# Performance work log

Measured on AMD Instinct MI355X. Metric: run time of the kernel, lower is better.

Reference implementation:

```python
import jax, jax.numpy as jnp
import numpy as np

NEG_SLOPE = 0.01  # F.leaky_relu default


def gcn_conv(x, src, dst, norm, W, b, n_nodes):
    """PyG-style GCNConv: h = x @ W; out[i] = sum_{(j->i)} norm_e * h[j] + b.
    src/dst/norm already include self-loops and symmetric D^-1/2 A D^-1/2 weights."""
    h = x @ W                                   # [N, out]
    msgs = h[src] * norm[:, None]               # [E+N, out] gather
    out = jax.ops.segment_sum(msgs, dst, num_segments=n_nodes)  # scatter-add
    return out + b


def _build_norm(edge_idx, n_nodes):
    """Add self-loops and compute symmetric GCN normalization coefficients."""
    loops = jnp.arange(n_nodes, dtype=edge_idx.dtype)
    src = jnp.concatenate([edge_idx[0], loops])
    dst = jnp.concatenate([edge_idx[1], loops])
    deg = jax.ops.segment_sum(jnp.ones_like(dst, dtype=jnp.float32), dst,
                              num_segments=n_nodes)
    dinv = jnp.where(deg > 0, jax.lax.rsqrt(jnp.maximum(deg, 1.0)), 0.0)
    norm = dinv[src] * dinv[dst]
    return src, dst, norm


def setup_inputs() -> dict:
    key = jax.random.key(0)
    k = jax.random.split(key, 8)
    N, E, nfeat, nhid = 50000, 800000, 64, 64
    x = jax.random.normal(k[0], (N, nfeat), dtype=jnp.float32)
    edge_idx = jax.random.randint(k[1], (2, E), 0, N, dtype=jnp.int32)
    # inverted dropout mask, p=0.5 -> values in {0, 2}
    drop_mask = (jax.random.uniform(k[2], (N, nhid)) >= 0.5).astype(jnp.float32) * 2.0
    # glorot-style GCNConv weights + zero bias (PyG defaults)
    s1 = (6.0 / (nfeat + nhid)) ** 0.5
    s2 = (6.0 / (nhid + nhid // 2)) ** 0.5
    W1 = jax.random.uniform(k[3], (nfeat, nhid), minval=-s1, maxval=s1, dtype=jnp.float32)
    b1 = jnp.zeros((nhid,), dtype=jnp.float32)
    W2 = jax.random.uniform(k[4], (nhid, nhid // 2), minval=-s2, maxval=s2, dtype=jnp.float32)
    b2 = jnp.zeros((nhid // 2,), dtype=jnp.float32)
    return {"x": x, "edge_idx": edge_idx, "drop_mask": drop_mask,
            "W1": W1, "b1": b1, "W2": W2, "b2": b2}


def reference(x, edge_idx, drop_mask, W1, b1, W2, b2):
    n_nodes = x.shape[0]
    src, dst, norm = _build_norm(edge_idx, n_nodes)
    h = jax.nn.leaky_relu(gcn_conv(x, src, dst, norm, W1, b1, n_nodes), NEG_SLOPE)
    h = h * drop_mask  # F.dropout(p=0.5) with precomputed inverted mask
    out = jax.nn.leaky_relu(gcn_conv(h, src, dst, norm, W2, b2, n_nodes), NEG_SLOPE)
    return out
```

## Files before the change

kernel.cpp:

```cpp
#include <hip/hip_runtime.h>
#include <hip/hip_fp16.h>

#define NEG_SLOPE 0.01f
typedef unsigned int uint;
typedef unsigned short u16;

#define NBK 256
#define CHUNK 4096
#define KPT 16
#define GROWS 16

__device__ __forceinline__ float wbits(uint rec) {
    u16 b = (u16)(rec >> 16);
    __half h;
    *reinterpret_cast<u16*>(&h) = b;
    return __half2float(h);
}

__device__ __forceinline__ void acc8(uint4 v, float w, float* a) {
    float2 f;
    f = __half22float2(*reinterpret_cast<__half2*>(&v.x)); a[0] = fmaf(f.x, w, a[0]); a[1] = fmaf(f.y, w, a[1]);
    f = __half22float2(*reinterpret_cast<__half2*>(&v.y)); a[2] = fmaf(f.x, w, a[2]); a[3] = fmaf(f.y, w, a[3]);
    f = __half22float2(*reinterpret_cast<__half2*>(&v.z)); a[4] = fmaf(f.x, w, a[4]); a[5] = fmaf(f.y, w, a[5]);
    f = __half22float2(*reinterpret_cast<__half2*>(&v.w)); a[6] = fmaf(f.x, w, a[6]); a[7] = fmaf(f.y, w, a[7]);
}

__device__ __forceinline__ void unpack8(uint4 v, float* s) {
    float2 f;
    f = __half22float2(*reinterpret_cast<__half2*>(&v.x)); s[0] = f.x; s[1] = f.y;
    f = __half22float2(*reinterpret_cast<__half2*>(&v.y)); s[2] = f.x; s[3] = f.y;
    f = __half22float2(*reinterpret_cast<__half2*>(&v.z)); s[4] = f.x; s[5] = f.y;
    f = __half22float2(*reinterpret_cast<__half2*>(&v.w)); s[6] = f.x; s[7] = f.y;
}

__global__ __launch_bounds__(256) void gemm1_hist(const float* __restrict__ X,
                                                  const float* __restrict__ W,
                                                  __half* __restrict__ H, int N,
                                                  const int* __restrict__ dst,
                                                  uint* __restrict__ hist, int E,
                                                  int gblocks) {
    __shared__ uint lh[NBK];
    if ((int)blockIdx.x >= gblocks) {
        int cb = (int)blockIdx.x - gblocks;
        int t = threadIdx.x;
        lh[t] = 0u;
        __syncthreads();
        int base = cb * CHUNK;
#pragma unroll
        for (int r = 0; r < 4; ++r) {
            int e4 = base + r * 1024 + t * 4;
            if (e4 + 3 < E) {
                int4 d = *(const int4*)(dst + e4);
                atomicAdd(&lh[((uint)d.x) >> 8], 1u);
                atomicAdd(&lh[((uint)d.y) >> 8], 1u);
                atomicAdd(&lh[((uint)d.z) >> 8], 1u);
                atomicAdd(&lh[((uint)d.w) >> 8], 1u);
            } else {
                for (int e = e4; e < E && e < e4 + 4; ++e)
                    atomicAdd(&lh[((uint)dst[e]) >> 8], 1u);
            }
        }
        __syncthreads();
        hist[(size_t)cb * NBK + t] = lh[t];
        return;
    }
    int lane = threadIdx.x & 63;
    int wv = threadIdx.x >> 6;
    float wc[64];
#pragma unroll
    for (int k = 0; k < 64; ++k) wc[k] = W[k * 64 + lane];
    size_t plane = (size_t)(lane >> 5) * ((size_t)N * 32);
    int c = lane & 31;
    int rowBase = ((int)blockIdx.x * 4 + wv) * GROWS;
    for (int g = 0; g < GROWS; g += 4) {
        int r0 = __builtin_amdgcn_readfirstlane(rowBase + g);
        if (r0 >= N) return;
        int e1 = min(r0 + 1, N - 1), e2 = min(r0 + 2, N - 1), e3 = min(r0 + 3, N - 1);
        const float* x0 = X + (size_t)r0 * 64;
        const float* x1 = X + (size_t)e1 * 64;
        const float* x2 = X + (size_t)e2 * 64;
        const float* x3 = X + (size_t)e3 * 64;
        float a0 = 0.f, a1 = 0.f, a2 = 0.f, a3 = 0.f;
        float b0 = 0.f, b1 = 0.f, b2 = 0.f, b3 = 0.f;
#pragma unroll
        for (int k = 0; k < 64; k += 2) {
            a0 = fmaf(x0[k], wc[k], a0); b0 = fmaf(x0[k + 1], wc[k + 1], b0);
            a1 = fmaf(x1[k], wc[k], a1); b1 = fmaf(x1[k + 1], wc[k + 1], b1);
            a2 = fmaf(x2[k], wc[k], a2); b2 = fmaf(x2[k + 1], wc[k + 1], b2);
            a3 = fmaf(x3[k], wc[k], a3); b3 = fmaf(x3[k + 1], wc[k + 1], b3);
        }
        H[plane + (size_t)r0 * 32 + c] = __float2half(a0 + b0);
        if (r0 + 1 < N) H[plane + (size_t)(r0 + 1) * 32 + c] = __float2half(a1 + b1);
        if (r0 + 2 < N) H[plane + (size_t)(r0 + 2) * 32 + c] = __float2half(a2 + b2);
        if (r0 + 3 < N) H[plane + (size_t)(r0 + 3) * 32 + c] = __float2half(a3 + b3);
    }
}

__global__ __launch_bounds__(256) void scan_hist(uint* __restrict__ hist,
                                                 uint* __restrict__ buckTotal,
                                                 int nchunks) {
    __shared__ uint lds[256];
    int b = blockIdx.x;
    int t = threadIdx.x;
    uint carry = 0;
    for (int c0 = 0; c0 < nchunks; c0 += 256) {
        int c = c0 + t;
        uint v = (c < nchunks) ? hist[(size_t)c * NBK + b] : 0u;
        lds[t] = v;
        __syncthreads();
        for (int off = 1; off < 256; off <<= 1) {
            uint u = (t >= off) ? lds[t - off] : 0u;
            __syncthreads();
            lds[t] += u;
            __syncthreads();
        }
        uint incl = lds[t];
        if (c < nchunks) hist[(size_t)c * NBK + b] = carry + incl - v;
        uint tot = lds[255];
        __syncthreads();
        carry += tot;
    }
    if (t == 0) buckTotal[b] = carry;
}

__global__ __launch_bounds__(256) void partition_edges(const int* __restrict__ src,
                                                       const int* __restrict__ dst,
                                                       const uint* __restrict__ hist,
                                                       const uint* __restrict__ buckTotal,
                                                       uint* __restrict__ staging,
                                                       int E) {
    __shared__ uint lh[NBK];
    __shared__ uint sc[NBK];
    __shared__ uint runbase[NBK];
    int t = threadIdx.x;
    lh[t] = 0u;
    uint tot = buckTotal[t];
    sc[t] = tot;
    __syncthreads();
    for (int off = 1; off < NBK; off <<= 1) {
        uint u = (t >= off) ? sc[t - off] : 0u;
        __syncthreads();
        sc[t] += u;
        __syncthreads();
    }
    int base = blockIdx.x * CHUNK;
    uint rec[KPT], rb[KPT], rk[KPT];
#pragma unroll
    for (int r = 0; r < 4; ++r) {
        int e4 = base + r * 1024 + t * 4;
        if (e4 + 3 < E) {
            int4 s = *(const int4*)(src + e4);
            int4 d = *(const int4*)(dst + e4);
            int k = r * 4;
            rb[k + 0] = ((uint)d.x) >> 8; rec[k + 0] = (uint)s.x | (((uint)d.x & 255u) << 16);
            rb[k + 1] = ((uint)d.y) >> 8; rec[k + 1] = (uint)s.y | (((uint)d.y & 255u) << 16);
            rb[k + 2] = ((uint)d.z) >> 8; rec[k + 2] = (uint)s.z | (((uint)d.z & 255u) << 16);
            rb[k + 3] = ((uint)d.w) >> 8; rec[k + 3] = (uint)s.w | (((uint)d.w & 255u) << 16);
            rk[k + 0] = atomicAdd(&lh[rb[k + 0]], 1u);
            rk[k + 1] = atomicAdd(&lh[rb[k + 1]], 1u);
            rk[k + 2] = atomicAdd(&lh[rb[k + 2]], 1u);
            rk[k + 3] = atomicAdd(&lh[rb[k + 3]], 1u);
        } else {
            for (int j = 0; j < 4; ++j) {
                int e = e4 + j;
                int k = r * 4 + j;
                if (e < E) {
                    uint s = (uint)src[e], d = (uint)dst[e];
                    rb[k] = d >> 8;
                    rec[k] = s | ((d & 255u) << 16);
                    rk[k] = atomicAdd(&lh[rb[k]], 1u);
                } else rb[k] = 0xFFFFFFFFu;
            }
        }
    }
    __syncthreads();
    runbase[t] = (sc[t] - tot) + hist[(size_t)blockIdx.x * NBK + t];
    __syncthreads();
#pragma unroll
    for (int k = 0; k < KPT; ++k)
        if (rb[k] != 0xFFFFFFFFu)
            staging[runbase[rb[k]] + rk[k]] = rec[k];
}

__global__ __launch_bounds__(256) void build_csr(const uint* __restrict__ staging,
                                                 const uint* __restrict__ buckTotal,
                                                 u16* __restrict__ srcIdx,
                                                 uint* __restrict__ offs,
                                                 float* __restrict__ dinv,
                                                 int N, int nbuck) {
    __shared__ uint nh[256];
    __shared__ uint nstart[256];
    __shared__ u16 rankbuf[8192];
    __shared__ u16 outbuf[8192];
    int b = blockIdx.x;
    int t = threadIdx.x;
    uint tot = buckTotal[t];
    nstart[t] = tot;
    __syncthreads();
    for (int off = 1; off < NBK; off <<= 1) {
        uint u = (t >= off) ? nstart[t - off] : 0u;
        __syncthreads();
        nstart[t] += u;
        __syncthreads();
    }
    uint endb = nstart[b];
    uint base = endb - buckTotal[b];
    __syncthreads();
    uint T = endb - base;
    nh[t] = 0u;
    __syncthreads();
    for (uint i = t; i < T; i += 256) {
        uint rec = staging[base + i];
        rankbuf[i] = (u16)atomicAdd(&nh[(rec >> 16) & 255u], 1u);
    }
    __syncthreads();
    uint deg = nh[t];
    nstart[t] = deg;
    __syncthreads();
    for (int off = 1; off < 256; off <<= 1) {
        uint u = (t >= off) ? nstart[t - off] : 0u;
        __syncthreads();
        nstart[t] += u;
        __syncthreads();
    }
    uint excl = nstart[t] - deg;
    __syncthreads();
    nstart[t] = excl;
    __syncthreads();
    for (uint i = t; i < T; i += 256) {
        uint rec = staging[base + i];
        outbuf[nstart[(rec >> 16) & 255u] + rankbuf[i]] = (u16)(rec & 0xFFFFu);
    }
    __syncthreads();
    for (uint i = t; i < T; i += 256) srcIdx[base + i] = outbuf[i];
    int node = b * 256 + t;
    if (node < N) {
        offs[node] = base + excl;
        dinv[node] = rsqrtf((float)(deg + 1u));
    }
    if (b == nbuck - 1 && t == 0) offs[N] = endb;
}

__global__ __launch_bounds__(256) void fill_pack(const u16* __restrict__ srcIdx,
                                                 const float* __restrict__ dinv,
                                                 uint* __restrict__ packed, int E) {
    int i4 = (blockIdx.x * 256 + threadIdx.x) * 4;
    if (i4 + 3 < E) {
        ushort4 s = *(const ushort4*)(srcIdx + i4);
        uint4 o;
        __half h0 = __float2half(dinv[s.x]);
        __half h1 = __float2half(dinv[s.y]);
        __half h2 = __float2half(dinv[s.z]);
        __half h3 = __float2half(dinv[s.w]);
        o.x = (uint)s.x | ((uint)*reinterpret_cast<u16*>(&h0) << 16);
        o.y = (uint)s.y | ((uint)*reinterpret_cast<u16*>(&h1) << 16);
        o.z = (uint)s.z | ((uint)*reinterpret_cast<u16*>(&h2) << 16);
        o.w = (uint)s.w | ((uint)*reinterpret_cast<u16*>(&h3) << 16);
        *(uint4*)(packed + i4) = o;
    } else {
        for (int i = i4; i < E; ++i) {
            __half h = __float2half(dinv[srcIdx[i]]);
            packed[i] = (uint)srcIdx[i] | ((uint)*reinterpret_cast<u16*>(&h) << 16);
        }
    }
}

__global__ __launch_bounds__(256) void agg1(const __half* __restrict__ h,
                                            const uint* __restrict__ offs,
                                            const uint* __restrict__ packed,
                                            const float* __restrict__ dinv,
                                            const float* __restrict__ b,
                                            const float* __restrict__ mask,
                                            __half* __restrict__ outp,
                                            int N, int nb1) {
    int half = ((int)blockIdx.x >= nb1) ? 1 : 0;
    int blk = (int)blockIdx.x - half * nb1;
    int node = blk * 4 + (threadIdx.x >> 6);
    if (node >= N) return;
    int lane = threadIdx.x & 63;
    int r = lane >> 2;
    int q = lane & 3;
    const uint4* h8 = (const uint4*)(h + (size_t)half * N * 32);
    uint beg = offs[node], end = offs[node + 1];
    float a[8] = {0.f, 0.f, 0.f, 0.f, 0.f, 0.f, 0.f, 0.f};
    uint p = beg + (uint)r;
    for (; p + 16 < end; p += 32) {
        uint e0 = packed[p], e1 = packed[p + 16];
        uint4 v0 = h8[(size_t)(e0 & 0xFFFFu) * 4 + q];
        uint4 v1 = h8[(size_t)(e1 & 0xFFFFu) * 4 + q];
        acc8(v0, wbits(e0), a);
        acc8(v1, wbits(e1), a);
    }
    for (; p < end; p += 16) {
        uint e0 = packed[p];
        uint4 v0 = h8[(size_t)(e0 & 0xFFFFu) * 4 + q];
        acc8(v0, wbits(e0), a);
    }
#pragma unroll
    for (int i = 0; i < 8; ++i) {
        a[i] += __shfl_xor(a[i], 4, 64);
        a[i] += __shfl_xor(a[i], 8, 64);
        a[i] += __shfl_xor(a[i], 16, 64);
        a[i] += __shfl_xor(a[i], 32, 64);
    }
    if (r == 0) {
        float dv = dinv[node];
        float dv2 = dv * dv;
        float s[8];
        unpack8(h8[(size_t)node * 4 + q], s);
        const float4* b4 = (const float4*)b;
        float4 bv0 = b4[half * 8 + q * 2];
        float4 bv1 = b4[half * 8 + q * 2 + 1];
        const float4* m4 = (const float4*)mask;
        float4 mv0 = m4[(size_t)node * 16 + half * 8 + q * 2];
        float4 mv1 = m4[(size_t)node * 16 + half * 8 + q * 2 + 1];
        float bb[8] = {bv0.x, bv0.y, bv0.z, bv0.w, bv1.x, bv1.y, bv1.z, bv1.w};
        float mm[8] = {mv0.x, mv0.y, mv0.z, mv0.w, mv1.x, mv1.y, mv1.z, mv1.w};
        uint4 o;
        uint* op = (uint*)&o;
#pragma unroll
        for (int i = 0; i < 4; ++i) {
            float v0 = a[2 * i] * dv + s[2 * i] * dv2 + bb[2 * i];
            float v1 = a[2 * i + 1] * dv + s[2 * i + 1] * dv2 + bb[2 * i + 1];
            v0 = (v0 > 0.f) ? v0 : NEG_SLOPE * v0;
            v1 = (v1 > 0.f) ? v1 : NEG_SLOPE * v1;
            v0 *= mm[2 * i]; v1 *= mm[2 * i + 1];
            __half2 hh = __floats2half2_rn(v0, v1);
            op[i] = *reinterpret_cast<uint*>(&hh);
        }
        ((uint4*)(outp + (size_t)half * N * 32))[(size_t)node * 4 + q] = o;
    }
}

__global__ __launch_bounds__(256) void gemm64x32(const __half* __restrict__ Xh,
                                                 const float* __restrict__ W,
                                                 __half* __restrict__ H, int N) {
    int lane = threadIdx.x & 63;
    int col = lane & 31;
    int wv = threadIdx.x >> 6;
    size_t N32 = (size_t)N * 32;
    float wc[64];
#pragma unroll
    for (int k = 0; k < 64; ++k) wc[k] = W[k * 32 + col];
    int rowBase = ((int)blockIdx.x * 4 + wv) * GROWS;
    for (int g = 0; g < GROWS; g += 4) {
        int r0 = __builtin_amdgcn_readfirstlane(rowBase + g);
        if (r0 >= N) return;
        int e1 = min(r0 + 1, N - 1), e2 = min(r0 + 2, N - 1), e3 = min(r0 + 3, N - 1);
        float a0 = 0.f, a1 = 0.f, a2 = 0.f, a3 = 0.f;
        float b0 = 0.f, b1 = 0.f, b2 = 0.f, b3 = 0.f;
#pragma unroll
        for (int pl = 0; pl < 2; ++pl) {
            const uint* x0 = (const uint*)(Xh + pl * N32 + (size_t)r0 * 32);
            const uint* x1 = (const uint*)(Xh + pl * N32 + (size_t)e1 * 32);
            const uint* x2 = (const uint*)(Xh + pl * N32 + (size_t)e2 * 32);
            const uint* x3 = (const uint*)(Xh + pl * N32 + (size_t)e3 * 32);
#pragma unroll
            for (int kk = 0; kk < 16; ++kk) {
                uint u0 = x0[kk], u1 = x1[kk], u2 = x2[kk], u3 = x3[kk];
                float2 f0 = __half22float2(*reinterpret_cast<__half2*>(&u0));
                float2 f1 = __half22float2(*reinterpret_cast<__half2*>(&u1));
                float2 f2 = __half22float2(*reinterpret_cast<__half2*>(&u2));
                float2 f3 = __half22float2(*reinterpret_cast<__half2*>(&u3));
                int k0 = pl * 32 + 2 * kk;
                a0 = fmaf(f0.x, wc[k0], a0); b0 = fmaf(f0.y, wc[k0 + 1], b0);
                a1 = fmaf(f1.x, wc[k0], a1); b1 = fmaf(f1.y, wc[k0 + 1], b1);
                a2 = fmaf(f2.x, wc[k0], a2); b2 = fmaf(f2.y, wc[k0 + 1], b2);
                a3 = fmaf(f3.x, wc[k0], a3); b3 = fmaf(f3.y, wc[k0 + 1], b3);
            }
        }
        if (lane < 32) {
            H[(size_t)r0 * 32 + col] = __float2half(a0 + b0);
            if (r0 + 1 < N) H[(size_t)(r0 + 1) * 32 + col] = __float2half(a1 + b1);
            if (r0 + 2 < N) H[(size_t)(r0 + 2) * 32 + col] = __float2half(a2 + b2);
            if (r0 + 3 < N) H[(size_t)(r0 + 3) * 32 + col] = __float2half(a3 + b3);
        }
    }
}

__global__ __launch_bounds__(256) void agg2(const __half* __restrict__ h,
                                            const uint* __restrict__ offs,
                                            const uint* __restrict__ packed,
                                            const float* __restrict__ dinv,
                                            const float* __restrict__ b,
                                            float* __restrict__ outp, int N) {
    int node = (int)blockIdx.x * 4 + (threadIdx.x >> 6);
    if (node >= N) return;
    int lane = threadIdx.x & 63;
    int r = lane >> 2;
    int q = lane & 3;
    const uint4* h8 = (const uint4*)h;
    uint beg = offs[node], end = offs[node + 1];
    float a[8] = {0.f, 0.f, 0.f, 0.f, 0.f, 0.f, 0.f, 0.f};
    uint p = beg + (uint)r;
    for (; p + 16 < end; p += 32) {
        uint e0 = packed[p], e1 = packed[p + 16];
        uint4 v0 = h8[(size_t)(e0 & 0xFFFFu) * 4 + q];
        uint4 v1 = h8[(size_t)(e1 & 0xFFFFu) * 4 + q];
        acc8(v0, wbits(e0), a);
        acc8(v1, wbits(e1), a);
    }
    for (; p < end; p += 16) {
        uint e0 = packed[p];
        uint4 v0 = h8[(size_t)(e0 & 0xFFFFu) * 4 + q];
        acc8(v0, wbits(e0), a);
    }
#pragma unroll
    for (int i = 0; i < 8; ++i) {
        a[i] += __shfl_xor(a[i], 4, 64);
        a[i] += __shfl_xor(a[i], 8, 64);
        a[i] += __shfl_xor(a[i], 16, 64);
        a[i] += __shfl_xor(a[i], 32, 64);
    }
    if (r == 0) {
        float dv = dinv[node];
        float dv2 = dv * dv;
        float s[8];
        unpack8(h8[(size_t)node * 4 + q], s);
        float4 bv0 = ((const float4*)b)[q * 2];
        float4 bv1 = ((const float4*)b)[q * 2 + 1];
        float bb[8] = {bv0.x, bv0.y, bv0.z, bv0.w, bv1.x, bv1.y, bv1.z, bv1.w};
        float o[8];
#pragma unroll
        for (int i = 0; i < 8; ++i) {
            float v = a[i] * dv + s[i] * dv2 + bb[i];
            o[i] = (v > 0.f) ? v : NEG_SLOPE * v;
        }
        float4* outv = (float4*)outp;
        outv[(size_t)node * 8 + q * 2]     = make_float4(o[0], o[1], o[2], o[3]);
        outv[(size_t)node * 8 + q * 2 + 1] = make_float4(o[4], o[5], o[6], o[7]);
    }
}

extern "C" void kernel_launch(void* const* d_in, const int* in_sizes, int n_in,
                              void* d_out, int out_size, void* d_ws, size_t ws_size,
                              hipStream_t stream) {
    const float* x    = (const float*)d_in[0];
    const int*   ei   = (const int*)d_in[1];
    const float* mask = (const float*)d_in[2];
    const float* W1   = (const float*)d_in[3];
    const float* b1   = (const float*)d_in[4];
    const float* W2   = (const float*)d_in[5];
    const float* b2   = (const float*)d_in[6];
    float* out = (float*)d_out;

    const int N = in_sizes[0] / 64;
    const int E = in_sizes[1] / 2;
    const int* src = ei;
    const int* dst = ei + E;

    const int nbuck  = (N + 255) >> 8;
    const int chunks = (E + CHUNK - 1) / CHUNK;
    const int gblocks = (N + 4 * GROWS - 1) / (4 * GROWS);
    const int nb1 = (N + 3) / 4;

    char* w = (char*)d_ws;
    uint*  hist      = (uint*)w;    w += (size_t)chunks * NBK * 4;
    uint*  buckTotal = (uint*)w;    w += NBK * 4;
    w = (char*)(((size_t)w + 15) & ~15ull);
    uint*  offs      = (uint*)w;    w += (size_t)(N + 1) * 4;
    w = (char*)(((size_t)w + 15) & ~15ull);
    float* dinv      = (float*)w;   w += (size_t)N * 4;
    uint*  staging   = (uint*)w;    w += (size_t)E * 4;
    u16*   srcIdx    = (u16*)w;     w += (((size_t)E * 2 + 15) & ~15ull);
    uint*  packed    = (uint*)w;    w += (size_t)E * 4;
    __half* h1       = (__half*)w;  w += (size_t)N * 64 * 2;
    __half* hpost    = (__half*)w;  w += (size_t)N * 64 * 2;
    __half* h2       = h1;

    gemm1_hist<<<gblocks + chunks, 256, 0, stream>>>(x, W1, h1, N, dst, hist, E, gblocks);
    scan_hist<<<NBK, 256, 0, stream>>>(hist, buckTotal, chunks);
    partition_edges<<<chunks, 256, 0, stream>>>(src, dst, hist, buckTotal, staging, E);
    build_csr<<<nbuck, 256, 0, stream>>>(staging, buckTotal, srcIdx, offs, dinv, N, nbuck);
    fill_pack<<<(E + 1023) / 1024, 256, 0, stream>>>(srcIdx, dinv, packed, E);

    agg1<<<2 * nb1, 256, 0, stream>>>(h1, offs, packed, dinv, b1, mask, hpost, N, nb1);

    gemm64x32<<<gblocks, 256, 0, stream>>>(hpost, W2, h2, N);
    agg2<<<nb1, 256, 0, stream>>>(h2, offs, packed, dinv, b2, out, N);
}
```

Measured before the change: 137.1 us.

## Assign one node per 4-lane group in aggregation kernels instead of per wavefront

Both aggregation kernels now map each 4-lane group to one destination node, so a wavefront handles 16 nodes, where before one wavefront covered a single node. Each group walks its node's edge list sequentially with 4-way unrolled gathers, and the cross-lane shuffle reduction is gone. The goal is to stop wasting lanes, since average degree is about 17, so the 16-edge-strided loop left many lanes idle, and to remove the reduction overhead. In exchange, lanes in a wavefront diverge when their nodes have different degrees, and gather coalescing changes.

Measured after the change: 116.0 us (median of 2 runs). 1.18x faster.

```diff
diff --git a/kernel.cpp b/kernel.cpp
--- a/kernel.cpp
+++ b/kernel.cpp
@@ -272,48 +272,47 @@
                                             const float* __restrict__ b,
                                             const float* __restrict__ mask,
                                             __half* __restrict__ outp,
-                                            int N, int nb1) {
-    int half = ((int)blockIdx.x >= nb1) ? 1 : 0;
-    int blk = (int)blockIdx.x - half * nb1;
-    int node = blk * 4 + (threadIdx.x >> 6);
-    if (node >= N) return;
+                                            int N, int nbA) {
+    int pl = ((int)blockIdx.x >= nbA) ? 1 : 0;
+    int blk = (int)blockIdx.x - pl * nbA;
     int lane = threadIdx.x & 63;
-    int r = lane >> 2;
+    int wid = threadIdx.x >> 6;
+    int g = lane >> 2;
     int q = lane & 3;
-    const uint4* h8 = (const uint4*)(h + (size_t)half * N * 32);
-    uint beg = offs[node], end = offs[node + 1];
+    int node = blk * 64 + wid * 16 + g;
+    bool valid = node < N;
+    uint beg = 0, end = 0;
+    if (valid) { beg = offs[node]; end = offs[node + 1]; }
+    const uint4* h8 = (const uint4*)(h + (size_t)pl * N * 32);
     float a[8] = {0.f, 0.f, 0.f, 0.f, 0.f, 0.f, 0.f, 0.f};
-    uint p = beg + (uint)r;
-    for (; p + 16 < end; p += 32) {
-        uint e0 = packed[p], e1 = packed[p + 16];
+    uint p = beg;
+    for (; p + 3 < end; p += 4) {
+        uint e0 = packed[p], e1 = packed[p + 1], e2 = packed[p + 2], e3 = packed[p + 3];
         uint4 v0 = h8[(size_t)(e0 & 0xFFFFu) * 4 + q];
         uint4 v1 = h8[(size_t)(e1 & 0xFFFFu) * 4 + q];
+        uint4 v2 = h8[(size_t)(e2 & 0xFFFFu) * 4 + q];
+        uint4 v3 = h8[(size_t)(e3 & 0xFFFFu) * 4 + q];
         acc8(v0, wbits(e0), a);
         acc8(v1, wbits(e1), a);
-    }
-    for (; p < end; p += 16) {
+        acc8(v2, wbits(e2), a);
+        acc8(v3, wbits(e3), a);
+    }
+    for (; p < end; ++p) {
         uint e0 = packed[p];
         uint4 v0 = h8[(size_t)(e0 & 0xFFFFu) * 4 + q];
         acc8(v0, wbits(e0), a);
     }
-#pragma unroll
-    for (int i = 0; i < 8; ++i) {
-        a[i] += __shfl_xor(a[i], 4, 64);
-        a[i] += __shfl_xor(a[i], 8, 64);
-        a[i] += __shfl_xor(a[i], 16, 64);
-        a[i] += __shfl_xor(a[i], 32, 64);
-    }
-    if (r == 0) {
+    if (valid) {
         float dv = dinv[node];
         float dv2 = dv * dv;
         float s[8];
         unpack8(h8[(size_t)node * 4 + q], s);
         const float4* b4 = (const float4*)b;
-        float4 bv0 = b4[half * 8 + q * 2];
-        float4 bv1 = b4[half * 8 + q * 2 + 1];
+        float4 bv0 = b4[pl * 8 + q * 2];
+        float4 bv1 = b4[pl * 8 + q * 2 + 1];
         const float4* m4 = (const float4*)mask;
-        float4 mv0 = m4[(size_t)node * 16 + half * 8 + q * 2];
-        float4 mv1 = m4[(size_t)node * 16 + half * 8 + q * 2 + 1];
+        float4 mv0 = m4[(size_t)node * 16 + pl * 8 + q * 2];
+        float4 mv1 = m4[(size_t)node * 16 + pl * 8 + q * 2 + 1];
         float bb[8] = {bv0.x, bv0.y, bv0.z, bv0.w, bv1.x, bv1.y, bv1.z, bv1.w};
         float mm[8] = {mv0.x, mv0.y, mv0.z, mv0.w, mv1.x, mv1.y, mv1.z, mv1.w};
         uint4 o;
@@ -328,7 +327,7 @@
             __half2 hh = __floats2half2_rn(v0, v1);
             op[i] = *reinterpret_cast<uint*>(&hh);
         }
-        ((uint4*)(outp + (size_t)half * N * 32))[(size_t)node * 4 + q] = o;
+        ((uint4*)(outp + (size_t)pl * N * 32))[(size_t)node * 4 + q] = o;
     }
 }
 
@@ -384,35 +383,34 @@
                                             const float* __restrict__ dinv,
                                             const float* __restrict__ b,
                                             float* __restrict__ outp, int N) {
-    int node = (int)blockIdx.x * 4 + (threadIdx.x >> 6);
-    if (node >= N) return;
     int lane = threadIdx.x & 63;
-    int r = lane >> 2;
+    int wid = threadIdx.x >> 6;
+    int g = lane >> 2;
     int q = lane & 3;
+    int node = (int)blockIdx.x * 64 + wid * 16 + g;
+    bool valid = node < N;
+    uint beg = 0, end = 0;
+    if (valid) { beg = offs[node]; end = offs[node + 1]; }
     const uint4* h8 = (const uint4*)h;
-    uint beg = offs[node], end = offs[node + 1];
     float a[8] = {0.f, 0.f, 0.f, 0.f, 0.f, 0.f, 0.f, 0.f};
-    uint p = beg + (uint)r;
-    for (; p + 16 < end; p += 32) {
-        uint e0 = packed[p], e1 = packed[p + 16];
+    uint p = beg;
+    for (; p + 3 < end; p += 4) {
+        uint e0 = packed[p], e1 = packed[p + 1], e2 = packed[p + 2], e3 = packed[p + 3];
         uint4 v0 = h8[(size_t)(e0 & 0xFFFFu) * 4 + q];
         uint4 v1 = h8[(size_t)(e1 & 0xFFFFu) * 4 + q];
+        uint4 v2 = h8[(size_t)(e2 & 0xFFFFu) * 4 + q];
+        uint4 v3 = h8[(size_t)(e3 & 0xFFFFu) * 4 + q];
         acc8(v0, wbits(e0), a);
         acc8(v1, wbits(e1), a);
-    }
-    for (; p < end; p += 16) {
+        acc8(v2, wbits(e2), a);
+        acc8(v3, wbits(e3), a);
+    }
+    for (; p < end; ++p) {
         uint e0 = packed[p];
         uint4 v0 = h8[(size_t)(e0 & 0xFFFFu) * 4 + q];
         acc8(v0, wbits(e0), a);
     }
-#pragma unroll
-    for (int i = 0; i < 8; ++i) {
-        a[i] += __shfl_xor(a[i], 4, 64);
-        a[i] += __shfl_xor(a[i], 8, 64);
-        a[i] += __shfl_xor(a[i], 16, 64);
-        a[i] += __shfl_xor(a[i], 32, 64);
-    }
-    if (r == 0) {
+    if (valid) {
         float dv = dinv[node];
         float dv2 = dv * dv;
         float s[8];
@@ -452,7 +450,7 @@
     const int nbuck  = (N + 255) >> 8;
     const int chunks = (E + CHUNK - 1) / CHUNK;
     const int gblocks = (N + 4 * GROWS - 1) / (4 * GROWS);
-    const int nb1 = (N + 3) / 4;
+    const int nbA = (N + 63) / 64;
 
     char* w = (char*)d_ws;
     uint*  hist      = (uint*)w;    w += (size_t)chunks * NBK * 4;
@@ -474,8 +472,8 @@
     build_csr<<<nbuck, 256, 0, stream>>>(staging, buckTotal, srcIdx, offs, dinv, N, nbuck);
     fill_pack<<<(E + 1023) / 1024, 256, 0, stream>>>(srcIdx, dinv, packed, E);
 
-    agg1<<<2 * nb1, 256, 0, stream>>>(h1, offs, packed, dinv, b1, mask, hpost, N, nb1);
+    agg1<<<2 * nbA, 256, 0, stream>>>(h1, offs, packed, dinv, b1, mask, hpost, N, nbA);
 
     gemm64x32<<<gblocks, 256, 0, stream>>>(hpost, W2, h2, N);
-    agg2<<<nb1, 256, 0, stream>>>(h2, offs, packed, dinv, b2, out, N);
-}
+    agg2<<<nbA, 256, 0, stream>>>(h2, offs, packed, dinv, b2, out, N);
+}
```
